# Kernel optimization log

Hardware: AMD Instinct MI355X
Metric: run time of the kernel (lower is better)

The kernel has to match this reference:

```python
import jax, jax.numpy as jnp
import numpy as np

B, L, HID = 1, 2048, 4096
H, KV, D = 32, 2, 128
ROT = int(D * 0.5)  # partial rotary dims per head
THETA = 10000.0
SCALE = D ** -0.5


def _rope_tables(L, rot, theta):
    inv_freq = 1.0 / (theta ** (np.arange(0, rot, 2, dtype=np.float32) / rot))  # [rot/2]
    t = np.arange(L, dtype=np.float32)
    freqs = np.outer(t, inv_freq)  # [L, rot/2]
    return jnp.asarray(np.cos(freqs)), jnp.asarray(np.sin(freqs))


def setup_inputs() -> dict:
    key = jax.random.key(0)
    ks = jax.random.split(key, 8)
    s = HID ** -0.5
    x = jax.random.normal(ks[0], (B, L, HID), dtype=jnp.float32)
    Wq = jax.random.normal(ks[1], (HID, H * D), dtype=jnp.float32) * s
    Wk = jax.random.normal(ks[2], (HID, KV * D), dtype=jnp.float32) * s
    Wv = jax.random.normal(ks[3], (HID, KV * D), dtype=jnp.float32) * s
    Wo = jax.random.normal(ks[4], (H * D, HID), dtype=jnp.float32) * s
    bq = jax.random.normal(ks[5], (H * D,), dtype=jnp.float32) * 0.01
    bk = jax.random.normal(ks[6], (KV * D,), dtype=jnp.float32) * 0.01
    bv = jax.random.normal(ks[7], (KV * D,), dtype=jnp.float32) * 0.01
    cos, sin = _rope_tables(L, ROT, THETA)
    # additive causal mask
    causal = jnp.tril(jnp.ones((L, L), dtype=bool))
    attention_mask = jnp.where(causal, 0.0, -1e9)[None, None].astype(jnp.float32)
    return {"x": x, "Wq": Wq, "bq": bq, "Wk": Wk, "bk": bk, "Wv": Wv, "bv": bv,
            "Wo": Wo, "cos": cos, "sin": sin, "attention_mask": attention_mask}


def _apply_rope(t, cos, sin):
    # t: [B, h, L, D]; rotary on first ROT dims, pass-through on the rest
    t_rot, t_pass = t[..., :ROT], t[..., ROT:]
    x1, x2 = t_rot[..., : ROT // 2], t_rot[..., ROT // 2:]
    c = cos[None, None]  # [1,1,L,ROT/2]
    s = sin[None, None]
    rot = jnp.concatenate([x1 * c - x2 * s, x2 * c + x1 * s], axis=-1)
    return jnp.concatenate([rot, t_pass], axis=-1)


def reference(x, Wq, bq, Wk, bk, Wv, bv, Wo, cos, sin, attention_mask):
    Bx, Lx, _ = x.shape
    q = (x @ Wq + bq).reshape(Bx, Lx, H, D).transpose(0, 2, 1, 3)   # [B,H,L,D]
    k = (x @ Wk + bk).reshape(Bx, Lx, KV, D).transpose(0, 2, 1, 3)  # [B,KV,L,D]
    v = (x @ Wv + bv).reshape(Bx, Lx, KV, D).transpose(0, 2, 1, 3)
    q = _apply_rope(q, cos, sin)
    k = _apply_rope(k, cos, sin)
    # GQA: repeat KV heads
    rep = H // KV
    k = jnp.repeat(k, rep, axis=1)  # [B,H,L,D]
    v = jnp.repeat(v, rep, axis=1)
    w = jnp.einsum('bhqd,bhkd->bhqk', q, k) * SCALE + attention_mask
    w = jax.nn.softmax(w, axis=-1)
    o = jnp.einsum('bhqk,bhkd->bhqd', w, v)
    o = o.transpose(0, 2, 1, 3).reshape(Bx, Lx, H * D)
    return o @ Wo
```

## Files before the change

### kernel.cpp

```cpp
#include <hip/hip_runtime.h>
#include <stdint.h>

#define L_SEQ 2048
#define HID   4096
#define NH    32
#define NKV   2
#define DH    128
#define NQKV  4608
#define QSCALE 0.088388347648318447f

typedef __bf16 bf16x8 __attribute__((ext_vector_type(8)));
typedef float  f32x4  __attribute__((ext_vector_type(4)));

__device__ __forceinline__ unsigned short f2bf(float f) {
  union { float f; unsigned u; } cv; cv.f = f;
  unsigned u = cv.u;
  return (unsigned short)((u + 0x7fffu + ((u >> 16) & 1u)) >> 16);
}
__device__ __forceinline__ float bf2f(unsigned short h) {
  union { unsigned u; float f; } cv; cv.u = (unsigned)h << 16; return cv.f;
}
__device__ __forceinline__ unsigned pk2(float a, float b) {
  return (unsigned)f2bf(a) | ((unsigned)f2bf(b) << 16);
}

#define GLL16(gsrc, ldst)                                                              \
  __builtin_amdgcn_global_load_lds(                                                    \
      (const __attribute__((address_space(1))) unsigned int*)(gsrc),                   \
      (__attribute__((address_space(3))) unsigned int*)(ldst), 16, 0, 0)

__global__ __launch_bounds__(256) void cast_bf16_kernel(const float* __restrict__ in,
                                                        unsigned short* __restrict__ out,
                                                        int n4) {
  int i = blockIdx.x * 256 + threadIdx.x;
  if (i >= n4) return;
  float4 v = reinterpret_cast<const float4*>(in)[i];
  ushort4 o;
  o.x = f2bf(v.x); o.y = f2bf(v.y); o.z = f2bf(v.z); o.w = f2bf(v.w);
  reinterpret_cast<ushort4*>(out)[i] = o;
}

__global__ __launch_bounds__(256) void transpose_cast_kernel(const float* __restrict__ in,
                                                             unsigned short* __restrict__ out,
                                                             int R, int C) {
  __shared__ float tile[64][65];
  const int c0 = blockIdx.x * 64, r0 = blockIdx.y * 64;
  const int tid = threadIdx.x;
  #pragma unroll
  for (int it = 0; it < 4; ++it) {
    int row = it * 16 + (tid >> 4);
    float4 v = *reinterpret_cast<const float4*>(&in[(size_t)(r0 + row) * C + c0 + (tid & 15) * 4]);
    tile[row][(tid & 15) * 4 + 0] = v.x;
    tile[row][(tid & 15) * 4 + 1] = v.y;
    tile[row][(tid & 15) * 4 + 2] = v.z;
    tile[row][(tid & 15) * 4 + 3] = v.w;
  }
  __syncthreads();
  #pragma unroll
  for (int it = 0; it < 8; ++it) {
    int c  = it * 8 + (tid >> 5);
    int rp = tid & 31;
    unsigned u = (unsigned)f2bf(tile[2 * rp][c]) | ((unsigned)f2bf(tile[2 * rp + 1][c]) << 16);
    *reinterpret_cast<unsigned*>(&out[(size_t)(c0 + c) * R + r0 + 2 * rp]) = u;
  }
}

__global__ __launch_bounds__(256) void vtrans_kernel(const unsigned short* __restrict__ in,
                                                     unsigned short* __restrict__ out) {
  __shared__ unsigned short tile[64][72];
  const int l0 = blockIdx.x * 64, d0 = blockIdx.y * 64, g = blockIdx.z;
  const int tid = threadIdx.x;
  #pragma unroll
  for (int it = 0; it < 2; ++it) {
    int l = it * 32 + (tid >> 3);
    *reinterpret_cast<uint4*>(&tile[l][(tid & 7) * 8]) =
        *reinterpret_cast<const uint4*>(&in[((size_t)g * L_SEQ + l0 + l) * DH + d0 + (tid & 7) * 8]);
  }
  __syncthreads();
  #pragma unroll
  for (int it = 0; it < 2; ++it) {
    int d = it * 32 + (tid >> 3);
    unsigned short tmp[8];
    #pragma unroll
    for (int e = 0; e < 8; ++e) tmp[e] = tile[(tid & 7) * 8 + e][d];
    *reinterpret_cast<uint4*>(&out[((size_t)g * DH + d0 + d) * L_SEQ + l0 + (tid & 7) * 8]) =
        *reinterpret_cast<uint4*>(tmp);
  }
}

#define TBM 128
#define TBN 128
#define TBK 64

template <int MODE>
__global__ __launch_bounds__(256, 2) void gemm128_kernel(const unsigned short* __restrict__ A,
                                                         const unsigned short* __restrict__ Bt,
                                                         float* __restrict__ C,
                                                         const float* __restrict__ bq,
                                                         const float* __restrict__ bk,
                                                         const float* __restrict__ bv,
                                                         const float* __restrict__ cosT,
                                                         const float* __restrict__ sinT,
                                                         unsigned short* __restrict__ qb,
                                                         unsigned short* __restrict__ kb,
                                                         unsigned short* __restrict__ vlin,
                                                         int M, int N, int K) {
  __shared__ __attribute__((aligned(16))) unsigned short As[2][TBM * TBK];
  __shared__ __attribute__((aligned(16))) unsigned short Bs[2][TBN * TBK];
  const int tid = threadIdx.x;
  const int wave = tid >> 6, lane = tid & 63;
  const int lg = lane >> 4, ll = lane & 15;
  const int wm = wave >> 1, wn = wave & 1;

  int gx = gridDim.x, nwg = gx * gridDim.y;
  int flat = blockIdx.y * gx + blockIdx.x;
  int bx = blockIdx.x, by = blockIdx.y;
  if ((nwg & 7) == 0) {
    int t = (flat & 7) * (nwg >> 3) + (flat >> 3);
    bx = t % gx; by = t / gx;
  }
  const int m0 = by * TBM, n0 = bx * TBN;

  f32x4 acc[4][4] = {};
  const int NT = K >> 6;

  auto stage = [&](int t, int buf) {
    const int k0 = t * TBK;
    #pragma unroll
    for (int i = 0; i < 4; ++i) {
      int ci  = (i * 4 + wave) * 64 + lane;
      int row = ci >> 3;
      int cg  = (ci & 7) ^ (row & 7);
      GLL16(A + (size_t)(m0 + row) * K + k0 + cg * 8, &As[buf][(i * 4 + wave) * 512]);
    }
    #pragma unroll
    for (int i = 0; i < 4; ++i) {
      int ci  = (i * 4 + wave) * 64 + lane;
      int row = ci >> 3;
      int cg  = (ci & 7) ^ (row & 7);
      GLL16(Bt + (size_t)(n0 + row) * K + k0 + cg * 8, &Bs[buf][(i * 4 + wave) * 512]);
    }
  };

  stage(0, 0);
  stage(1, 1);

  for (int t = 0; t < NT; ++t) {
    const int cur = t & 1;
    if (t + 1 < NT) asm volatile("s_waitcnt vmcnt(8)" ::: "memory");
    else            asm volatile("s_waitcnt vmcnt(0)" ::: "memory");
    __builtin_amdgcn_s_barrier();

    const unsigned short* Ac = &As[cur][0];
    const unsigned short* Bc = &Bs[cur][0];
    bf16x8 afr[2][4], bfr[2][4];
    #pragma unroll
    for (int kk = 0; kk < 2; ++kk)
      #pragma unroll
      for (int i = 0; i < 4; ++i) {
        int ra = wm * 64 + i * 16 + ll;
        afr[kk][i] = *reinterpret_cast<const bf16x8*>(
            &Ac[ra * 64 + (((kk * 4 + lg) ^ (ra & 7)) * 8)]);
        int rb = wn * 64 + i * 16 + ll;
        bfr[kk][i] = *reinterpret_cast<const bf16x8*>(
            &Bc[rb * 64 + (((kk * 4 + lg) ^ (rb & 7)) * 8)]);
      }
    asm volatile("s_waitcnt lgkmcnt(0)" ::: "memory");
    __builtin_amdgcn_s_barrier();
    if (t + 2 < NT) stage(t + 2, cur);

    __builtin_amdgcn_s_setprio(1);
    #pragma unroll
    for (int kk = 0; kk < 2; ++kk)
      #pragma unroll
      for (int i = 0; i < 4; ++i)
        #pragma unroll
        for (int j = 0; j < 4; ++j)
          acc[i][j] = __builtin_amdgcn_mfma_f32_16x16x32_bf16(afr[kk][i], bfr[kk][j],
                                                              acc[i][j], 0, 0, 0);
    __builtin_amdgcn_s_setprio(0);
  }

  if (MODE == 0) {
    #pragma unroll
    for (int i = 0; i < 4; ++i)
      #pragma unroll
      for (int j = 0; j < 4; ++j) {
        int col  = n0 + wn * 64 + j * 16 + ll;
        int rowb = m0 + wm * 64 + i * 16 + lg * 4;
        #pragma unroll
        for (int r = 0; r < 4; ++r)
          C[(size_t)(rowb + r) * N + col] = acc[i][j][r];
      }
  } else {
    const int region = (n0 < 4096) ? 0 : ((n0 < 4352) ? 1 : 2);
    const int hh = (region == 0) ? (n0 >> 7) : ((region == 1) ? ((n0 - 4096) >> 7) : ((n0 - 4352) >> 7));
    const float* bias = (region == 0) ? bq : ((region == 1) ? bk : bv);
    #pragma unroll
    for (int j = 0; j < 4; ++j) {
      float bj = bias[hh * DH + wn * 64 + j * 16 + ll];
      #pragma unroll
      for (int i = 0; i < 4; ++i)
        #pragma unroll
        for (int r = 0; r < 4; ++r) acc[i][j][r] += bj;
    }
    if (region < 2 && wn == 0) {
      #pragma unroll
      for (int i = 0; i < 4; ++i)
        #pragma unroll
        for (int r = 0; r < 4; ++r) {
          int l = m0 + wm * 64 + i * 16 + lg * 4 + r;
          float c0 = cosT[l * 32 + ll],      s0 = sinT[l * 32 + ll];
          float c1 = cosT[l * 32 + 16 + ll], s1 = sinT[l * 32 + 16 + ll];
          float x10 = acc[i][0][r], x20 = acc[i][2][r];
          float x11 = acc[i][1][r], x21 = acc[i][3][r];
          acc[i][0][r] = x10 * c0 - x20 * s0;
          acc[i][2][r] = x20 * c0 + x10 * s0;
          acc[i][1][r] = x11 * c1 - x21 * s1;
          acc[i][3][r] = x21 * c1 + x11 * s1;
        }
    }
    const float scale = (region == 0) ? QSCALE : 1.f;
    unsigned short* dst = (region == 0) ? qb : ((region == 1) ? kb : vlin);
    #pragma unroll
    for (int i = 0; i < 4; ++i)
      #pragma unroll
      for (int j = 0; j < 4; ++j) {
        int d = wn * 64 + j * 16 + ll;
        #pragma unroll
        for (int r = 0; r < 4; ++r) {
          int l = m0 + wm * 64 + i * 16 + lg * 4 + r;
          dst[((size_t)hh * L_SEQ + l) * DH + d] = f2bf(acc[i][j][r] * scale);
        }
      }
  }
}

__global__ __launch_bounds__(256, 2) void attn_kernel(const unsigned short* __restrict__ qg,
                                                      const unsigned short* __restrict__ kb,
                                                      const unsigned short* __restrict__ vt,
                                                      unsigned short* __restrict__ ob) {
  __shared__ __attribute__((aligned(16))) unsigned short Ks[2][64 * 128];
  __shared__ __attribute__((aligned(16))) unsigned short Vs[2][128 * 64];

  const int pair = blockIdx.x, h = blockIdx.y;
  const int g = h >> 4;
  const int tid = threadIdx.x, wave = tid >> 6, lane = tid & 63;
  const int lg = lane >> 4, ll = lane & 15;

  const int krow = (lane >> 4);
  const int kcg0 = (lane & 15);
  const int vrow = (lane >> 3);
  const int vcg0 = (lane & 7);

  #pragma unroll
  for (int seg = 0; seg < 2; ++seg) {
    const int qt = seg ? (31 - pair) : pair;
    const int q0 = qt * 64 + wave * 16;

    bf16x8 qf[4];
    #pragma unroll
    for (int f = 0; f < 4; ++f)
      qf[f] = *reinterpret_cast<const bf16x8*>(
          qg + ((size_t)h * L_SEQ + q0 + ll) * DH + f * 32 + lg * 8);

    f32x4 of[8] = {};
    float m = -1e30f, lsum = 0.f;

    const int kvN = qt + 1;
    int cur = 0;

    #pragma unroll
    for (int c = 0; c < 4; ++c) {
      int issue = wave * 4 + c;
      int rk = issue * 4 + krow;
      GLL16(kb + ((size_t)g * L_SEQ + rk) * DH + (kcg0 ^ (rk & 7)) * 8, &Ks[0][issue * 512]);
      int rv = issue * 8 + vrow;
      GLL16(vt + ((size_t)g * DH + rv) * L_SEQ + (vcg0 ^ (rv & 7)) * 8, &Vs[0][issue * 512]);
    }
    __syncthreads();

    for (int t = 0; t < kvN; ++t) {
      if (t + 1 < kvN) {
        int kv1 = (t + 1) * 64;
        #pragma unroll
        for (int c = 0; c < 4; ++c) {
          int issue = wave * 4 + c;
          int rk = issue * 4 + krow;
          GLL16(kb + ((size_t)g * L_SEQ + kv1 + rk) * DH + (kcg0 ^ (rk & 7)) * 8,
                &Ks[cur ^ 1][issue * 512]);
          int rv = issue * 8 + vrow;
          GLL16(vt + ((size_t)g * DH + rv) * L_SEQ + kv1 + (vcg0 ^ (rv & 7)) * 8,
                &Vs[cur ^ 1][issue * 512]);
        }
      }

      f32x4 s[4] = {};
      const unsigned short* Kc = &Ks[cur][0];
      #pragma unroll
      for (int cf = 0; cf < 4; ++cf) {
        bf16x8 kf[4];
        #pragma unroll
        for (int f = 0; f < 4; ++f) {
          int rk = cf * 16 + ll;
          int cc = (f * 4 + lg) ^ (rk & 7);
          kf[f] = *reinterpret_cast<const bf16x8*>(&Kc[rk * 128 + cc * 8]);
        }
        __builtin_amdgcn_s_setprio(1);
        #pragma unroll
        for (int f = 0; f < 4; ++f)
          s[cf] = __builtin_amdgcn_mfma_f32_16x16x32_bf16(kf[f], qf[f], s[cf], 0, 0, 0);
        __builtin_amdgcn_s_setprio(0);
      }

      if (t == qt) {
        #pragma unroll
        for (int cf = 0; cf < 4; ++cf)
          #pragma unroll
          for (int r = 0; r < 4; ++r)
            if (cf * 16 + lg * 4 + r > wave * 16 + ll) s[cf][r] = -1e30f;
      }

      float pmax = -1e30f;
      #pragma unroll
      for (int cf = 0; cf < 4; ++cf)
        #pragma unroll
        for (int r = 0; r < 4; ++r) pmax = fmaxf(pmax, s[cf][r]);
      if (!__all(pmax - m <= 8.f)) {
        float mx = fmaxf(pmax, __shfl_xor(pmax, 16));
        mx = fmaxf(mx, __shfl_xor(mx, 32));
        float mnew = fmaxf(m, mx);
        float alpha = __expf(m - mnew);
        m = mnew;
        lsum *= alpha;
        float af[4];
        #pragma unroll
        for (int r = 0; r < 4; ++r) af[r] = __shfl(alpha, lg * 4 + r);
        #pragma unroll
        for (int ds = 0; ds < 8; ++ds)
          #pragma unroll
          for (int r = 0; r < 4; ++r) of[ds][r] *= af[r];
      }

      unsigned wlo[4], whi[4];
      float psum = 0.f;
      #pragma unroll
      for (int cf = 0; cf < 4; ++cf) {
        float p0 = __expf(s[cf][0] - m), p1 = __expf(s[cf][1] - m);
        float p2 = __expf(s[cf][2] - m), p3 = __expf(s[cf][3] - m);
        psum += (p0 + p1) + (p2 + p3);
        wlo[cf] = pk2(p0, p1);
        whi[cf] = pk2(p2, p3);
      }
      lsum += psum;

      bf16x8 pa[2];
      {
        const int src0 = ((lg & 1) << 5) + ll;
        const int src1 = src0 + 16;
        const bool hi = (lg & 2) != 0;
        #pragma unroll
        for (int ks = 0; ks < 2; ++ks) {
          int e0a = __shfl((int)wlo[ks * 2], src0);
          int e1a = __shfl((int)whi[ks * 2], src0);
          int e2a = __shfl((int)wlo[ks * 2], src1);
          int e3a = __shfl((int)whi[ks * 2], src1);
          int e0b = __shfl((int)wlo[ks * 2 + 1], src0);
          int e1b = __shfl((int)whi[ks * 2 + 1], src0);
          int e2b = __shfl((int)wlo[ks * 2 + 1], src1);
          int e3b = __shfl((int)whi[ks * 2 + 1], src1);
          union { int i[4]; bf16x8 v; } u;
          u.i[0] = hi ? e0b : e0a;
          u.i[1] = hi ? e1b : e1a;
          u.i[2] = hi ? e2b : e2a;
          u.i[3] = hi ? e3b : e3a;
          pa[ks] = u.v;
        }
      }

      const unsigned short* Vc = &Vs[cur][0];
      #pragma unroll
      for (int ds = 0; ds < 8; ++ds) {
        bf16x8 vf[2];
        #pragma unroll
        for (int ks = 0; ks < 2; ++ks) {
          int dl = ds * 16 + ll;
          int cc = (ks * 4 + lg) ^ (dl & 7);
          vf[ks] = *reinterpret_cast<const bf16x8*>(&Vc[dl * 64 + cc * 8]);
        }
        __builtin_amdgcn_s_setprio(1);
        #pragma unroll
        for (int ks = 0; ks < 2; ++ks)
          of[ds] = __builtin_amdgcn_mfma_f32_16x16x32_bf16(pa[ks], vf[ks], of[ds], 0, 0, 0);
        __builtin_amdgcn_s_setprio(0);
      }

      __syncthreads();
      cur ^= 1;
    }

    float tot = lsum + __shfl_xor(lsum, 16);
    tot += __shfl_xor(tot, 32);
    float inv = 1.f / tot;
    float invr[4];
    #pragma unroll
    for (int r = 0; r < 4; ++r) invr[r] = __shfl(inv, lg * 4 + r);
    #pragma unroll
    for (int ds = 0; ds < 8; ++ds)
      #pragma unroll
      for (int r = 0; r < 4; ++r) {
        int row = q0 + lg * 4 + r;
        ob[(size_t)row * (NH * DH) + h * DH + ds * 16 + ll] = f2bf(of[ds][r] * invr[r]);
      }
    __syncthreads();
  }
}

extern "C" void kernel_launch(void* const* d_in, const int* in_sizes, int n_in,
                              void* d_out, int out_size, void* d_ws, size_t ws_size,
                              hipStream_t stream) {
  (void)in_sizes; (void)n_in; (void)out_size; (void)ws_size;
  const float* x    = (const float*)d_in[0];
  const float* Wq   = (const float*)d_in[1];
  const float* bq   = (const float*)d_in[2];
  const float* Wk   = (const float*)d_in[3];
  const float* bk   = (const float*)d_in[4];
  const float* Wv   = (const float*)d_in[5];
  const float* bv   = (const float*)d_in[6];
  const float* Wo   = (const float*)d_in[7];
  const float* cosT = (const float*)d_in[8];
  const float* sinT = (const float*)d_in[9];

  char* ws = (char*)d_ws;
  size_t off = 0;
  auto alloc = [&](size_t bytes) { void* p = ws + off; off += (bytes + 255) & ~(size_t)255; return p; };
  unsigned short* xb    = (unsigned short*)alloc((size_t)L_SEQ * HID * 2);
  unsigned short* Wqkvt = (unsigned short*)alloc((size_t)NQKV * HID * 2);
  unsigned short* Wot   = (unsigned short*)alloc((size_t)HID * HID * 2);
  unsigned short* qbuf  = (unsigned short*)alloc((size_t)NH * L_SEQ * DH * 2);
  unsigned short* kbuf  = (unsigned short*)alloc((size_t)NKV * L_SEQ * DH * 2);
  unsigned short* vlin  = (unsigned short*)alloc((size_t)NKV * L_SEQ * DH * 2);
  unsigned short* vtb   = (unsigned short*)alloc((size_t)NKV * DH * L_SEQ * 2);
  unsigned short* attno = (unsigned short*)alloc((size_t)L_SEQ * HID * 2);

  cast_bf16_kernel<<<(L_SEQ * HID / 4 + 255) / 256, 256, 0, stream>>>(x, xb, L_SEQ * HID / 4);
  transpose_cast_kernel<<<dim3(HID / 64, HID / 64), 256, 0, stream>>>(Wq, Wqkvt, HID, HID);
  transpose_cast_kernel<<<dim3(256 / 64, HID / 64), 256, 0, stream>>>(Wk, Wqkvt + (size_t)4096 * HID, HID, 256);
  transpose_cast_kernel<<<dim3(256 / 64, HID / 64), 256, 0, stream>>>(Wv, Wqkvt + (size_t)4352 * HID, HID, 256);
  transpose_cast_kernel<<<dim3(HID / 64, HID / 64), 256, 0, stream>>>(Wo, Wot, HID, HID);

  gemm128_kernel<1><<<dim3(NQKV / TBN, L_SEQ / TBM), 256, 0, stream>>>(
      xb, Wqkvt, nullptr, bq, bk, bv, cosT, sinT, qbuf, kbuf, vlin, L_SEQ, NQKV, HID);

  vtrans_kernel<<<dim3(L_SEQ / 64, DH / 64, NKV), 256, 0, stream>>>(vlin, vtb);

  attn_kernel<<<dim3(16, NH), 256, 0, stream>>>(qbuf, kbuf, vtb, attno);

  gemm128_kernel<0><<<dim3(HID / TBN, L_SEQ / TBM), 256, 0, stream>>>(
      attno, Wot, (float*)d_out, nullptr, nullptr, nullptr, nullptr, nullptr,
      nullptr, nullptr, nullptr, L_SEQ, HID, HID);
}
```

Measured before the change: 316.5 us.

## Replace 128x128 GEMM with 256x256 8-wave tile and staged sub-tile pipeline

The projection GEMMs move from 128x128 tiles on 256 threads to 256x256 tiles on 512 threads (8 waves, each computing 128x64). The K=64 step is split into 32-wide halves with four staged load units interleaved between MFMA phases, using a new 4-way LDS swizzle and sched barriers to overlap global-to-LDS copies with compute. The goal is more data reuse per loaded byte and less exposed memory latency. The cost is fewer workgroups (144 for QKV, 128 for the output projection, on a 256-CU device), which leaves many CUs idle, plus higher register pressure from 32 accumulators per wave.

```diff
diff --git a/kernel.cpp b/kernel.cpp
--- a/kernel.cpp
+++ b/kernel.cpp
@@ -28,6 +28,8 @@
   __builtin_amdgcn_global_load_lds(                                                    \
       (const __attribute__((address_space(1))) unsigned int*)(gsrc),                   \
       (__attribute__((address_space(3))) unsigned int*)(ldst), 16, 0, 0)
+
+#define SWZ(row) ((((row) ^ ((row) >> 2))) & 3)
 
 __global__ __launch_bounds__(256) void cast_bf16_kernel(const float* __restrict__ in,
                                                         unsigned short* __restrict__ out,
@@ -88,12 +90,8 @@
   }
 }
 
-#define TBM 128
-#define TBN 128
-#define TBK 64
-
 template <int MODE>
-__global__ __launch_bounds__(256, 2) void gemm128_kernel(const unsigned short* __restrict__ A,
+__global__ __launch_bounds__(512, 1) void gemm256_kernel(const unsigned short* __restrict__ A,
                                                          const unsigned short* __restrict__ Bt,
                                                          float* __restrict__ C,
                                                          const float* __restrict__ bq,
@@ -105,12 +103,12 @@
                                                          unsigned short* __restrict__ kb,
                                                          unsigned short* __restrict__ vlin,
                                                          int M, int N, int K) {
-  __shared__ __attribute__((aligned(16))) unsigned short As[2][TBM * TBK];
-  __shared__ __attribute__((aligned(16))) unsigned short Bs[2][TBN * TBK];
+  __shared__ __attribute__((aligned(16))) unsigned short As[2][2][256 * 32];
+  __shared__ __attribute__((aligned(16))) unsigned short Bs[2][2][256 * 32];
   const int tid = threadIdx.x;
   const int wave = tid >> 6, lane = tid & 63;
   const int lg = lane >> 4, ll = lane & 15;
-  const int wm = wave >> 1, wn = wave & 1;
+  const int wm = wave >> 2, wn = wave & 3;
 
   int gx = gridDim.x, nwg = gx * gridDim.y;
   int flat = blockIdx.y * gx + blockIdx.x;
@@ -119,97 +117,144 @@
     int t = (flat & 7) * (nwg >> 3) + (flat >> 3);
     bx = t % gx; by = t / gx;
   }
-  const int m0 = by * TBM, n0 = bx * TBN;
-
-  f32x4 acc[4][4] = {};
+  const int m0 = by * 256, n0 = bx * 256;
+
+  f32x4 acc[8][4] = {};
   const int NT = K >> 6;
 
-  auto stage = [&](int t, int buf) {
-    const int k0 = t * TBK;
-    #pragma unroll
-    for (int i = 0; i < 4; ++i) {
-      int ci  = (i * 4 + wave) * 64 + lane;
-      int row = ci >> 3;
-      int cg  = (ci & 7) ^ (row & 7);
-      GLL16(A + (size_t)(m0 + row) * K + k0 + cg * 8, &As[buf][(i * 4 + wave) * 512]);
-    }
-    #pragma unroll
-    for (int i = 0; i < 4; ++i) {
-      int ci  = (i * 4 + wave) * 64 + lane;
-      int row = ci >> 3;
-      int cg  = (ci & 7) ^ (row & 7);
-      GLL16(Bt + (size_t)(n0 + row) * K + k0 + cg * 8, &Bs[buf][(i * 4 + wave) * 512]);
+  const int srow0 = wave * 16 + (lane >> 2);
+  const int scg0  = lane & 3;
+
+  auto stage_unit = [&](int t, int u) {
+    const int r = t & 1, kh = u >> 1;
+    const unsigned short* src = (u & 1) ? Bt : A;
+    const int base0 = (u & 1) ? n0 : m0;
+    unsigned short* dst = (u & 1) ? &Bs[r][kh][0] : &As[r][kh][0];
+    #pragma unroll
+    for (int l = 0; l < 2; ++l) {
+      int row = l * 128 + srow0;
+      int cg  = scg0 ^ SWZ(row);
+      GLL16(src + (size_t)(base0 + row) * K + t * 64 + kh * 32 + cg * 8,
+            dst + (l * 512 + wave * 64) * 8);
     }
   };
 
-  stage(0, 0);
-  stage(1, 1);
-
-  for (int t = 0; t < NT; ++t) {
-    const int cur = t & 1;
-    if (t + 1 < NT) asm volatile("s_waitcnt vmcnt(8)" ::: "memory");
-    else            asm volatile("s_waitcnt vmcnt(0)" ::: "memory");
-    __builtin_amdgcn_s_barrier();
-
-    const unsigned short* Ac = &As[cur][0];
-    const unsigned short* Bc = &Bs[cur][0];
-    bf16x8 afr[2][4], bfr[2][4];
-    #pragma unroll
-    for (int kk = 0; kk < 2; ++kk)
-      #pragma unroll
-      for (int i = 0; i < 4; ++i) {
-        int ra = wm * 64 + i * 16 + ll;
-        afr[kk][i] = *reinterpret_cast<const bf16x8*>(
-            &Ac[ra * 64 + (((kk * 4 + lg) ^ (ra & 7)) * 8)]);
-        int rb = wn * 64 + i * 16 + ll;
-        bfr[kk][i] = *reinterpret_cast<const bf16x8*>(
-            &Bc[rb * 64 + (((kk * 4 + lg) ^ (rb & 7)) * 8)]);
-      }
+  auto rdA = [&](int r, int kh, int i) -> bf16x8 {
+    int row = wm * 128 + i * 16 + ll;
+    return *reinterpret_cast<const bf16x8*>(&As[r][kh][row * 32 + ((lg ^ SWZ(row)) * 8)]);
+  };
+  auto rdB = [&](int r, int kh, int j) -> bf16x8 {
+    int row = wn * 64 + j * 16 + ll;
+    return *reinterpret_cast<const bf16x8*>(&Bs[r][kh][row * 32 + ((lg ^ SWZ(row)) * 8)]);
+  };
+
+  auto tile = [&](int t, int r) {
+    const bool pf = (t + 1) < NT;
+    bf16x8 a[4], b[4];
+    if (pf) stage_unit(t + 1, 0);
+    #pragma unroll
+    for (int j = 0; j < 4; ++j) b[j] = rdB(r, 0, j);
+    #pragma unroll
+    for (int i = 0; i < 4; ++i) a[i] = rdA(r, 0, i);
+    __builtin_amdgcn_s_barrier();
     asm volatile("s_waitcnt lgkmcnt(0)" ::: "memory");
-    __builtin_amdgcn_s_barrier();
-    if (t + 2 < NT) stage(t + 2, cur);
-
+    __builtin_amdgcn_sched_barrier(0);
     __builtin_amdgcn_s_setprio(1);
     #pragma unroll
-    for (int kk = 0; kk < 2; ++kk)
-      #pragma unroll
-      for (int i = 0; i < 4; ++i)
-        #pragma unroll
-        for (int j = 0; j < 4; ++j)
-          acc[i][j] = __builtin_amdgcn_mfma_f32_16x16x32_bf16(afr[kk][i], bfr[kk][j],
-                                                              acc[i][j], 0, 0, 0);
+    for (int i = 0; i < 4; ++i)
+      #pragma unroll
+      for (int j = 0; j < 4; ++j)
+        acc[i][j] = __builtin_amdgcn_mfma_f32_16x16x32_bf16(a[i], b[j], acc[i][j], 0, 0, 0);
     __builtin_amdgcn_s_setprio(0);
+    __builtin_amdgcn_s_barrier();
+    if (pf) stage_unit(t + 1, 1);
+    #pragma unroll
+    for (int i = 0; i < 4; ++i) a[i] = rdA(r, 0, 4 + i);
+    __builtin_amdgcn_s_barrier();
+    asm volatile("s_waitcnt lgkmcnt(0)" ::: "memory");
+    __builtin_amdgcn_sched_barrier(0);
+    __builtin_amdgcn_s_setprio(1);
+    #pragma unroll
+    for (int i = 0; i < 4; ++i)
+      #pragma unroll
+      for (int j = 0; j < 4; ++j)
+        acc[4 + i][j] = __builtin_amdgcn_mfma_f32_16x16x32_bf16(a[i], b[j], acc[4 + i][j], 0, 0, 0);
+    __builtin_amdgcn_s_setprio(0);
+    if (pf) asm volatile("s_waitcnt vmcnt(4)" ::: "memory");
+    else    asm volatile("s_waitcnt vmcnt(0)" ::: "memory");
+    __builtin_amdgcn_s_barrier();
+    if (pf) stage_unit(t + 1, 2);
+    #pragma unroll
+    for (int j = 0; j < 4; ++j) b[j] = rdB(r, 1, j);
+    #pragma unroll
+    for (int i = 0; i < 4; ++i) a[i] = rdA(r, 1, i);
+    __builtin_amdgcn_s_barrier();
+    asm volatile("s_waitcnt lgkmcnt(0)" ::: "memory");
+    __builtin_amdgcn_sched_barrier(0);
+    __builtin_amdgcn_s_setprio(1);
+    #pragma unroll
+    for (int i = 0; i < 4; ++i)
+      #pragma unroll
+      for (int j = 0; j < 4; ++j)
+        acc[i][j] = __builtin_amdgcn_mfma_f32_16x16x32_bf16(a[i], b[j], acc[i][j], 0, 0, 0);
+    __builtin_amdgcn_s_setprio(0);
+    __builtin_amdgcn_s_barrier();
+    if (pf) stage_unit(t + 1, 3);
+    #pragma unroll
+    for (int i = 0; i < 4; ++i) a[i] = rdA(r, 1, 4 + i);
+    __builtin_amdgcn_s_barrier();
+    asm volatile("s_waitcnt lgkmcnt(0)" ::: "memory");
+    __builtin_amdgcn_sched_barrier(0);
+    __builtin_amdgcn_s_setprio(1);
+    #pragma unroll
+    for (int i = 0; i < 4; ++i)
+      #pragma unroll
+      for (int j = 0; j < 4; ++j)
+        acc[4 + i][j] = __builtin_amdgcn_mfma_f32_16x16x32_bf16(a[i], b[j], acc[4 + i][j], 0, 0, 0);
+    __builtin_amdgcn_s_setprio(0);
+    if (pf) asm volatile("s_waitcnt vmcnt(4)" ::: "memory");
+    __builtin_amdgcn_s_barrier();
+  };
+
+  stage_unit(0, 0); stage_unit(0, 1); stage_unit(0, 2); stage_unit(0, 3);
+  asm volatile("s_waitcnt vmcnt(4)" ::: "memory");
+  __builtin_amdgcn_s_barrier();
+
+  for (int tt = 0; tt < NT; tt += 2) {
+    tile(tt, 0);
+    tile(tt + 1, 1);
   }
 
   if (MODE == 0) {
     #pragma unroll
-    for (int i = 0; i < 4; ++i)
+    for (int i = 0; i < 8; ++i)
       #pragma unroll
       for (int j = 0; j < 4; ++j) {
         int col  = n0 + wn * 64 + j * 16 + ll;
-        int rowb = m0 + wm * 64 + i * 16 + lg * 4;
+        int rowb = m0 + wm * 128 + i * 16 + lg * 4;
         #pragma unroll
         for (int r = 0; r < 4; ++r)
           C[(size_t)(rowb + r) * N + col] = acc[i][j][r];
       }
   } else {
     const int region = (n0 < 4096) ? 0 : ((n0 < 4352) ? 1 : 2);
-    const int hh = (region == 0) ? (n0 >> 7) : ((region == 1) ? ((n0 - 4096) >> 7) : ((n0 - 4352) >> 7));
+    const int hh = ((region == 0) ? (n0 >> 7) : 0) + (wn >> 1);
+    const int dbase = (wn & 1) * 64;
     const float* bias = (region == 0) ? bq : ((region == 1) ? bk : bv);
     #pragma unroll
     for (int j = 0; j < 4; ++j) {
-      float bj = bias[hh * DH + wn * 64 + j * 16 + ll];
-      #pragma unroll
-      for (int i = 0; i < 4; ++i)
+      float bj = bias[hh * DH + dbase + j * 16 + ll];
+      #pragma unroll
+      for (int i = 0; i < 8; ++i)
         #pragma unroll
         for (int r = 0; r < 4; ++r) acc[i][j][r] += bj;
     }
-    if (region < 2 && wn == 0) {
-      #pragma unroll
-      for (int i = 0; i < 4; ++i)
+    if (region < 2 && (wn & 1) == 0) {
+      #pragma unroll
+      for (int i = 0; i < 8; ++i)
         #pragma unroll
         for (int r = 0; r < 4; ++r) {
-          int l = m0 + wm * 64 + i * 16 + lg * 4 + r;
+          int l = m0 + wm * 128 + i * 16 + lg * 4 + r;
           float c0 = cosT[l * 32 + ll],      s0 = sinT[l * 32 + ll];
           float c1 = cosT[l * 32 + 16 + ll], s1 = sinT[l * 32 + 16 + ll];
           float x10 = acc[i][0][r], x20 = acc[i][2][r];
@@ -223,13 +268,13 @@
     const float scale = (region == 0) ? QSCALE : 1.f;
     unsigned short* dst = (region == 0) ? qb : ((region == 1) ? kb : vlin);
     #pragma unroll
-    for (int i = 0; i < 4; ++i)
+    for (int i = 0; i < 8; ++i)
       #pragma unroll
       for (int j = 0; j < 4; ++j) {
-        int d = wn * 64 + j * 16 + ll;
+        int d = dbase + j * 16 + ll;
         #pragma unroll
         for (int r = 0; r < 4; ++r) {
-          int l = m0 + wm * 64 + i * 16 + lg * 4 + r;
+          int l = m0 + wm * 128 + i * 16 + lg * 4 + r;
           dst[((size_t)hh * L_SEQ + l) * DH + d] = f2bf(acc[i][j][r] * scale);
         }
       }
@@ -449,14 +494,14 @@
   transpose_cast_kernel<<<dim3(256 / 64, HID / 64), 256, 0, stream>>>(Wv, Wqkvt + (size_t)4352 * HID, HID, 256);
   transpose_cast_kernel<<<dim3(HID / 64, HID / 64), 256, 0, stream>>>(Wo, Wot, HID, HID);
 
-  gemm128_kernel<1><<<dim3(NQKV / TBN, L_SEQ / TBM), 256, 0, stream>>>(
+  gemm256_kernel<1><<<dim3(NQKV / 256, L_SEQ / 256), 512, 0, stream>>>(
       xb, Wqkvt, nullptr, bq, bk, bv, cosT, sinT, qbuf, kbuf, vlin, L_SEQ, NQKV, HID);
 
   vtrans_kernel<<<dim3(L_SEQ / 64, DH / 64, NKV), 256, 0, stream>>>(vlin, vtb);
 
   attn_kernel<<<dim3(16, NH), 256, 0, stream>>>(qbuf, kbuf, vtb, attno);
 
-  gemm128_kernel<0><<<dim3(HID / TBN, L_SEQ / TBM), 256, 0, stream>>>(
+  gemm256_kernel<0><<<dim3(HID / 256, L_SEQ / 256), 512, 0, stream>>>(
       attno, Wot, (float*)d_out, nullptr, nullptr, nullptr, nullptr, nullptr,
       nullptr, nullptr, nullptr, L_SEQ, HID, HID);
 }
```

New measurement: 420.2 us. 1.33x slower.
